# Kernel optimization log

Measured on AMD Instinct MI355X. Metric: run time of the kernel, lower is better.

Reference implementation:

```python
import jax, jax.numpy as jnp
import numpy as np

N, M, E, D = 100000, 20000, 1600000, 128


def setup_inputs() -> dict:
    key = jax.random.key(0)
    ks = jax.random.split(key, 14)
    s = 1.0 / np.sqrt(D)
    inp = {
        "x": jax.random.normal(ks[0], (N, D), jnp.float32),
        "in_src": jax.random.randint(ks[1], (E,), 0, N),
        "in_dst": jax.random.randint(ks[2], (E,), 0, M),
        "has_src": jax.random.randint(ks[3], (E,), 0, M),
        "has_dst": jax.random.randint(ks[4], (E,), 0, N),
        "W1": jax.random.normal(ks[5], (D, D), jnp.float32) * s,
        "b1": jnp.zeros((D,), jnp.float32),
        "an1": jax.random.normal(ks[6], (D, 1), jnp.float32) * s,
        "ae1": jax.random.normal(ks[7], (D, 1), jnp.float32) * s,
        "W2": jax.random.normal(ks[8], (D, D), jnp.float32) * s,
        "b2": jnp.zeros((D,), jnp.float32),
        "an2": jax.random.normal(ks[9], (D, 1), jnp.float32) * s,
        "ae2": jax.random.normal(ks[10], (D, 1), jnp.float32) * s,
    }
    return inp


def _hgat_layer(x, W, b, an, ae, in_src, in_dst, has_src, has_dst, activate):
    h = x @ W + b                       # [N, D] fc transform
    n_attn = h @ an                     # [N, 1] node attn scores
    # node -> hyperedge ('in' edges). h_e is unset at this point (local_scope),
    # so the hyperedge bias term is zero; e = attn[src].
    e = n_attn[in_src]                  # [E, 1]
    # source uses F.softmax(e, dim=0): GLOBAL softmax over all edges
    attn = jax.nn.softmax(e, axis=0)    # [E, 1]
    h_e = jax.ops.segment_sum(attn * h[in_src], in_dst, num_segments=M)  # [M, D]
    e_attn = h_e @ ae                   # [M, 1] hyperedge attn scores
    # hyperedge -> node ('has' edges): bias is node attn score at dst
    e2 = e_attn[has_src] + n_attn[has_dst]  # [E, 1]
    attn2 = jax.nn.softmax(e2, axis=0)      # global softmax over all edges
    h_n = jax.ops.segment_sum(attn2 * h_e[has_src], has_dst, num_segments=N)  # [N, D]
    return jax.nn.relu(h_n) if activate else h_n


def reference(x, in_src, in_dst, has_src, has_dst,
              W1, b1, an1, ae1, W2, b2, an2, ae2):
    # layer 1 (activation=relu), layer 2 (no activation); dropout in eval mode
    h = _hgat_layer(x, W1, b1, an1, ae1, in_src, in_dst, has_src, has_dst, True)
    h = _hgat_layer(h, W2, b2, an2, ae2, in_src, in_dst, has_src, has_dst, False)
    return h
```

## Files before the change

kernel.cpp:

```cpp
#include <hip/hip_runtime.h>
#include <hip/hip_bf16.h>
#include <math.h>
#include <type_traits>


typedef unsigned int u32;
typedef unsigned short u16;
typedef u16 u16x8 __attribute__((ext_vector_type(8)));
typedef short bf16x8 __attribute__((ext_vector_type(8)));
typedef float f32x4 __attribute__((ext_vector_type(4)));

#define NCONST 100000
#define MCONST 20000
#define ECONST 1600000
#define HCH2 32768
#define HBC 32
#define NCH_N 4

#define PBLK 256
#define PT 6250
#define SHB_IN 6
#define NBK_IN 313
#define SRCB_IN 17
#define SHB_HAS 8
#define NBK_HAS 391
#define SRCB_HAS 15

__device__ __forceinline__ u16 f2bf(float f) {
  u32 u = __float_as_uint(f);
  u += 0x7FFFu + ((u >> 16) & 1u);
  return (u16)(u >> 16);
}
__device__ __forceinline__ float bf2f(u16 b) {
  return __uint_as_float(((u32)b) << 16);
}

__global__ __launch_bounds__(256) void k_hpart2(const int* __restrict__ in_dst,
                                                const int* __restrict__ has_dst,
                                                const int* __restrict__ in_src,
                                                int* __restrict__ partial) {
  __shared__ int hc[HCH2];
  int y = blockIdx.y;
  const int* __restrict__ arr = (y == 0) ? in_dst : (y <= 4 ? has_dst : in_src);
  int lo = (y == 0) ? 0 : (y <= 4 ? (y - 1) * HCH2 : (y - 5) * HCH2);
  for (int i = threadIdx.x; i < HCH2; i += 256) hc[i] = 0;
  __syncthreads();
  int stride = gridDim.x * 256;
  int n4 = ECONST >> 2;
  const int4* a4 = (const int4*)arr;
  for (int i = blockIdx.x * 256 + threadIdx.x; i < n4; i += stride) {
    int4 v = a4[i];
    u32 a = (u32)(v.x - lo), b = (u32)(v.y - lo), c = (u32)(v.z - lo), d = (u32)(v.w - lo);
    if (a < HCH2) atomicAdd(&hc[a], 1);
    if (b < HCH2) atomicAdd(&hc[b], 1);
    if (c < HCH2) atomicAdd(&hc[c], 1);
    if (d < HCH2) atomicAdd(&hc[d], 1);
  }
  __syncthreads();
  int* out = partial + ((size_t)y * HBC + blockIdx.x) * HCH2;
  for (int i = threadIdx.x; i < HCH2; i += 256) out[i] = hc[i];
}

__global__ void k_scan1d(const int* __restrict__ partial, int nM, int nN,
                         int* __restrict__ off_in, int* __restrict__ off_has,
                         int* __restrict__ deg, int* __restrict__ bsum) {
  __shared__ int sd[256];
  int y = blockIdx.y;
  int n = y ? nN : nM;
  int rowbase = (y == 0) ? 0 : (y == 1 ? 1 : 5);
  int t = threadIdx.x;
  int base = blockIdx.x * 1024 + t * 4;
  int v[4];
#pragma unroll
  for (int k = 0; k < 4; ++k) {
    int j = base + k;
    int s = 0;
    if (j < n) {
      int chunk = j >> 15;
      int jl = j & (HCH2 - 1);
      const int* p = partial + ((size_t)(rowbase + chunk) * HBC) * HCH2 + jl;
#pragma unroll
      for (int b = 0; b < HBC; ++b) s += p[(size_t)b * HCH2];
    }
    v[k] = s;
  }
  if (y == 2) {
#pragma unroll
    for (int k = 0; k < 4; ++k)
      if (base + k < n) deg[base + k] = v[k];
    return;
  }
  int* off = y ? off_has : off_in;
  int* bs = bsum + y * 128;
  v[1] += v[0]; v[2] += v[1]; v[3] += v[2];
  int tot = v[3];
  sd[t] = tot;
  __syncthreads();
  for (int o = 1; o < 256; o <<= 1) {
    int x = (t >= o) ? sd[t - o] : 0;
    __syncthreads();
    sd[t] += x;
    __syncthreads();
  }
  int excl = sd[t] - tot;
#pragma unroll
  for (int k = 0; k < 4; ++k)
    if (base + k < n) off[base + k + 1] = v[k] + excl;
  if (t == 255) bs[blockIdx.x] = sd[255];
}

__global__ void k_scan2d(int* __restrict__ bsum, int nbM, int nbN) {
  __shared__ int sd[256];
  int* bs = bsum + blockIdx.x * 128;
  int nb = blockIdx.x ? nbN : nbM;
  int t = threadIdx.x;
  int v = (t < nb) ? bs[t] : 0;
  sd[t] = v;
  __syncthreads();
  for (int o = 1; o < 256; o <<= 1) {
    int x = (t >= o) ? sd[t - o] : 0;
    __syncthreads();
    sd[t] += x;
    __syncthreads();
  }
  if (t < nb) bs[t] = sd[t] - v;
}

__global__ void k_scan3d(int* __restrict__ off_in, int* __restrict__ off_has,
                         const int* __restrict__ bsum, int nM, int nN) {
  int y = blockIdx.y;
  int* off = y ? off_has : off_in;
  const int* bs = bsum + y * 128;
  int n = y ? nN : nM;
  int i = blockIdx.x * blockDim.x + threadIdx.x;
  int st = gridDim.x * blockDim.x;
  if (blockIdx.x == 0 && threadIdx.x == 0) off[0] = 0;
  for (; i < n; i += st) off[i + 1] += bs[i >> 10];
}

__global__ __launch_bounds__(256) void k_coarse(const int* __restrict__ in_dst,
                                                const int* __restrict__ has_dst,
                                                int* __restrict__ bb_in,
                                                int* __restrict__ bb_has) {
  __shared__ int h1[NBK_IN];
  __shared__ int h2[NBK_HAS];
  for (int i = threadIdx.x; i < NBK_IN; i += 256) h1[i] = 0;
  for (int i = threadIdx.x; i < NBK_HAS; i += 256) h2[i] = 0;
  __syncthreads();
  int c0 = blockIdx.x * PT, c1 = min(c0 + PT, ECONST);
  for (int i = c0 + threadIdx.x; i < c1; i += 256) {
    atomicAdd(&h1[in_dst[i] >> SHB_IN], 1);
    atomicAdd(&h2[has_dst[i] >> SHB_HAS], 1);
  }
  __syncthreads();
  int* o1 = bb_in + (size_t)blockIdx.x * NBK_IN;
  for (int i = threadIdx.x; i < NBK_IN; i += 256) o1[i] = h1[i];
  int* o2 = bb_has + (size_t)blockIdx.x * NBK_HAS;
  for (int i = threadIdx.x; i < NBK_HAS; i += 256) o2[i] = h2[i];
}

template <int NBUK, int SHB>
__device__ __forceinline__ void colscan_body(int* __restrict__ bb,
                                             const int* __restrict__ off, int segs,
                                             int* sd) {
  int b = blockIdx.x;
  if (b >= NBUK) return;
  int t = threadIdx.x;
  int v = bb[(size_t)t * NBUK + b];
  sd[t] = v;
  __syncthreads();
  for (int o = 1; o < 256; o <<= 1) {
    int x = (t >= o) ? sd[t - o] : 0;
    __syncthreads();
    sd[t] += x;
    __syncthreads();
  }
  bb[(size_t)t * NBUK + b] = sd[t] - v + off[min(b << SHB, segs)];
}

__global__ __launch_bounds__(256) void k_colscan2(int* __restrict__ bb_in,
                                                  const int* __restrict__ off_in,
                                                  int* __restrict__ bb_has,
                                                  const int* __restrict__ off_has) {
  __shared__ int sd[256];
  if (blockIdx.y == 0)
    colscan_body<NBK_IN, SHB_IN>(bb_in, off_in, MCONST, sd);
  else
    colscan_body<NBK_HAS, SHB_HAS>(bb_has, off_has, NCONST, sd);
}

template <int NBUK, int SHB, int SRCB>
__device__ __forceinline__ void stage_body(const int* __restrict__ dst,
                                           const int* __restrict__ srcv,
                                           const int* __restrict__ bb,
                                           int* __restrict__ ebuf, int* hist, int* loff,
                                           int* gbase, int* stg, int* sd) {
  int t = threadIdx.x;
  for (int i = t; i < NBUK; i += 256) hist[i] = 0;
  __syncthreads();
  int c0 = blockIdx.x * PT, c1 = min(c0 + PT, ECONST);
  for (int i = c0 + t; i < c1; i += 256) atomicAdd(&hist[dst[i] >> SHB], 1);
  __syncthreads();
  {
    int v0 = (2 * t < NBUK) ? hist[2 * t] : 0;
    int v1 = (2 * t + 1 < NBUK) ? hist[2 * t + 1] : 0;
    sd[t] = v0 + v1;
    __syncthreads();
    for (int o = 1; o < 256; o <<= 1) {
      int x = (t >= o) ? sd[t - o] : 0;
      __syncthreads();
      sd[t] += x;
      __syncthreads();
    }
    int excl = sd[t] - (v0 + v1);
    if (2 * t < NBUK) loff[2 * t] = excl;
    if (2 * t + 1 < NBUK) loff[2 * t + 1] = excl + v0;
  }
  __syncthreads();
  for (int i = t; i < NBUK; i += 256) {
    gbase[i] = bb[(size_t)blockIdx.x * NBUK + i];
    hist[i] = loff[i];
  }
  __syncthreads();
  for (int i = c0 + t; i < c1; i += 256) {
    int d = dst[i], s = srcv[i];
    int b = d >> SHB;
    int r = atomicAdd(&hist[b], 1);
    stg[r] = (b << 23) | ((d & ((1 << SHB) - 1)) << SRCB) | s;
  }
  __syncthreads();
  int tot = c1 - c0;
  for (int i = t; i < tot; i += 256) {
    int v = stg[i];
    int b = ((u32)v) >> 23;
    ebuf[gbase[b] + (i - loff[b])] = v & ((1 << 23) - 1);
  }
}

__global__ __launch_bounds__(256) void k_stage2(
    const int* __restrict__ in_dst, const int* __restrict__ in_src,
    const int* __restrict__ bb_in, int* __restrict__ ebuf_in,
    const int* __restrict__ has_dst, const int* __restrict__ has_src,
    const int* __restrict__ bb_has, int* __restrict__ ebuf_has) {
  __shared__ int hist[NBK_HAS];
  __shared__ int loff[NBK_HAS];
  __shared__ int gbase[NBK_HAS];
  __shared__ int stg[PT];
  __shared__ int sd[256];
  if (blockIdx.y == 0)
    stage_body<NBK_IN, SHB_IN, SRCB_IN>(in_dst, in_src, bb_in, ebuf_in, hist, loff, gbase,
                                        stg, sd);
  else
    stage_body<NBK_HAS, SHB_HAS, SRCB_HAS>(has_dst, has_src, bb_has, ebuf_has, hist, loff,
                                           gbase, stg, sd);
}

template <int SHB, int SRCB>
__device__ __forceinline__ void place_body(const int* __restrict__ off, int segs,
                                           const int* __restrict__ ebuf,
                                           int* __restrict__ csrc, int* cur) {
  const int NSEG = 1 << SHB;
  int seg0 = blockIdx.x << SHB;
  if (seg0 >= segs) return;
  int segN = min(seg0 + NSEG, segs);
  for (int i = threadIdx.x; i < segN - seg0; i += 256) cur[i] = off[seg0 + i];
  __syncthreads();
  int start = off[seg0], end = off[segN];
  for (int i = start + threadIdx.x; i < end; i += 256) {
    int v = ebuf[i];
    int dloc = ((u32)v) >> SRCB;
    int pos = atomicAdd(&cur[dloc], 1);
    csrc[pos] = v & ((1 << SRCB) - 1);
  }
}

__global__ __launch_bounds__(256) void k_place2(
    const int* __restrict__ off_in, const int* __restrict__ ebuf_in,
    int* __restrict__ csrc_in, const int* __restrict__ off_has,
    const int* __restrict__ ebuf_has, int* __restrict__ csrc_has) {
  __shared__ int cur[256];
  if (blockIdx.y == 0)
    place_body<SHB_IN, SRCB_IN>(off_in, MCONST, ebuf_in, csrc_in, cur);
  else
    place_body<SHB_HAS, SRCB_HAS>(off_has, NCONST, ebuf_has, csrc_has, cur);
}

__device__ __forceinline__ void merge_write(float m, float s, float2* __restrict__ pairs) {
  for (int o = 1; o < 64; o <<= 1) {
    float om = __shfl_xor(m, o, 64), os = __shfl_xor(s, o, 64);
    float nm = fmaxf(m, om);
    s = s * __expf(m - nm) + os * __expf(om - nm);
    m = nm;
  }
  __shared__ float sm[4], ss[4];
  int t = threadIdx.x;
  if ((t & 63) == 0) { sm[t >> 6] = m; ss[t >> 6] = s; }
  __syncthreads();
  if (t == 0) {
    for (int k = 1; k < 4; ++k) {
      float nm = fmaxf(m, sm[k]);
      s = s * __expf(m - nm) + ss[k] * __expf(sm[k] - nm);
      m = nm;
    }
    pairs[blockIdx.x] = make_float2(m, s);
  }
}

template <typename IT>
__global__ __launch_bounds__(256, 3) void k_fc(
    const IT* __restrict__ x, const float* __restrict__ W,
    const float* __restrict__ bias, const float* __restrict__ an,
    const int* __restrict__ deg, u16* __restrict__ h, float* __restrict__ na,
    float2* __restrict__ pairs, int nrows) {
  __shared__ __align__(16) u16 sWT[128 * 136];
  __shared__ float sNa[128];
  int tid = threadIdx.x;
  int lane = tid & 63, w = tid >> 6;
  int cl = lane & 15, qg = lane >> 4;

  for (int i = tid * 4; i < 16384; i += 1024) {
    float4 v = *(const float4*)(W + i);
    int k = i >> 7, j = i & 127;
    sWT[(j + 0) * 136 + k] = f2bf(v.x);
    sWT[(j + 1) * 136 + k] = f2bf(v.y);
    sWT[(j + 2) * 136 + k] = f2bf(v.z);
    sWT[(j + 3) * 136 + k] = f2bf(v.w);
  }

  float anv[8], bv[8];
#pragma unroll
  for (int t = 0; t < 8; ++t) {
    anv[t] = an[t * 16 + cl];
    bv[t] = bias[t * 16 + cl];
  }

  int rbase = blockIdx.x * 128 + w * 32;
  bf16x8 afr[2][4];
#pragma unroll
  for (int g = 0; g < 2; ++g) {
    int r = rbase + g * 16 + cl;
    int rc = min(r, nrows - 1);
    const IT* xp = x + (size_t)rc * 128 + qg * 8;
#pragma unroll
    for (int s = 0; s < 4; ++s) {
      if constexpr (sizeof(IT) == 4) {
        float4 u0 = *(const float4*)(xp + s * 32);
        float4 u1 = *(const float4*)(xp + s * 32 + 4);
        bf16x8 a;
        a[0] = (short)f2bf(u0.x); a[1] = (short)f2bf(u0.y);
        a[2] = (short)f2bf(u0.z); a[3] = (short)f2bf(u0.w);
        a[4] = (short)f2bf(u1.x); a[5] = (short)f2bf(u1.y);
        a[6] = (short)f2bf(u1.z); a[7] = (short)f2bf(u1.w);
        afr[g][s] = a;
      } else {
        afr[g][s] = *(const bf16x8*)(xp + s * 32);
      }
    }
  }
  __syncthreads();

  f32x4 acc[2][8];
#pragma unroll
  for (int g = 0; g < 2; ++g)
#pragma unroll
    for (int t = 0; t < 8; ++t) {
      acc[g][t][0] = 0.f; acc[g][t][1] = 0.f; acc[g][t][2] = 0.f; acc[g][t][3] = 0.f;
    }

#pragma unroll
  for (int t = 0; t < 8; ++t) {
    bf16x8 bfrg[4];
    const u16* bp = sWT + (t * 16 + cl) * 136 + qg * 8;
#pragma unroll
    for (int s = 0; s < 4; ++s) bfrg[s] = *(const bf16x8*)(bp + s * 32);
#pragma unroll
    for (int s = 0; s < 4; ++s) {
#pragma unroll
      for (int g = 0; g < 2; ++g)
        acc[g][t] = __builtin_amdgcn_mfma_f32_16x16x32_bf16(afr[g][s], bfrg[s], acc[g][t],
                                                            0, 0, 0);
    }
  }

  float pa[2][4];
#pragma unroll
  for (int g = 0; g < 2; ++g)
#pragma unroll
    for (int reg = 0; reg < 4; ++reg) pa[g][reg] = 0.f;
#pragma unroll
  for (int g = 0; g < 2; ++g)
#pragma unroll
    for (int t = 0; t < 8; ++t)
#pragma unroll
      for (int reg = 0; reg < 4; ++reg)
        pa[g][reg] = fmaf(acc[g][t][reg] + bv[t], anv[t], pa[g][reg]);
#pragma unroll
  for (int g = 0; g < 2; ++g)
#pragma unroll
    for (int reg = 0; reg < 4; ++reg) {
      float v = pa[g][reg];
      v += __shfl_xor(v, 1, 64);
      v += __shfl_xor(v, 2, 64);
      v += __shfl_xor(v, 4, 64);
      v += __shfl_xor(v, 8, 64);
      pa[g][reg] = v;
    }
  if (cl == 0) {
#pragma unroll
    for (int g = 0; g < 2; ++g)
#pragma unroll
      for (int reg = 0; reg < 4; ++reg) {
        int r = rbase + g * 16 + qg * 4 + reg;
        int lidx = w * 32 + g * 16 + qg * 4 + reg;
        if (r < nrows) {
          na[r] = pa[g][reg];
          sNa[lidx] = pa[g][reg];
        }
      }
  }

  __syncthreads();
  u16* st = sWT + w * 32 * 136;
#pragma unroll
  for (int g = 0; g < 2; ++g)
#pragma unroll
    for (int t = 0; t < 8; ++t)
#pragma unroll
      for (int reg = 0; reg < 4; ++reg)
        st[(g * 16 + qg * 4 + reg) * 136 + t * 16 + cl] = f2bf(acc[g][t][reg] + bv[t]);
#pragma unroll
  for (int it = 0; it < 8; ++it) {
    int idx = it * 64 + lane;
    int row = idx >> 4, c = idx & 15;
    u16x8 v = *(const u16x8*)(st + row * 136 + c * 8);
    int r = rbase + row;
    if (r < nrows) *(u16x8*)(h + (size_t)r * 128 + c * 8) = v;
  }

  float m1 = -1e30f, s1 = 0.f;
  if (tid < 128) {
    int r = blockIdx.x * 128 + tid;
    if (r < nrows) {
      int d = deg[r];
      if (d > 0) { m1 = sNa[tid]; s1 = (float)d; }
    }
  }
  merge_write(m1, s1, pairs);
}

__global__ void k_sm2(const float* __restrict__ ea, const float* __restrict__ na,
                      const int* __restrict__ hs, const int* __restrict__ hd, int n,
                      float2* __restrict__ pairs) {
  float m = -1e30f, s = 0.f;
  int i = blockIdx.x * blockDim.x + threadIdx.x;
  int st = gridDim.x * blockDim.x;
  for (; i < n; i += st) {
    float xv = ea[hs[i]] + na[hd[i]];
    if (xv > m) { s *= __expf(m - xv); m = xv; }
    s += __expf(xv - m);
  }
  merge_write(m, s, pairs);
}

__global__ void k_smfin(const float2* __restrict__ pairs, int nb, float* __restrict__ out) {
  int t = threadIdx.x;
  float m = -1e30f, s = 0.f;
  for (int i = t; i < nb; i += 256) {
    float2 pr = pairs[i];
    float nm = fmaxf(m, pr.x);
    s = s * __expf(m - nm) + pr.y * __expf(pr.x - nm);
    m = nm;
  }
  for (int o = 1; o < 64; o <<= 1) {
    float om = __shfl_xor(m, o, 64), os = __shfl_xor(s, o, 64);
    float nm = fmaxf(m, om);
    s = s * __expf(m - nm) + os * __expf(om - nm);
    m = nm;
  }
  __shared__ float sm[4], ss[4];
  if ((t & 63) == 0) { sm[t >> 6] = m; ss[t >> 6] = s; }
  __syncthreads();
  if (t == 0) {
    for (int k = 1; k < 4; ++k) {
      float nm = fmaxf(m, sm[k]);
      s = s * __expf(m - nm) + ss[k] * __expf(sm[k] - nm);
      m = nm;
    }
    out[0] = m;
    out[1] = s;
  }
}

__global__ __launch_bounds__(256) void k_segA(
    const u16* __restrict__ h, const float* __restrict__ na,
    const float* __restrict__ scal, const int* __restrict__ csrc,
    const int* __restrict__ off, const float* __restrict__ ae, u16* __restrict__ he,
    float* __restrict__ ea, int m_count) {
  int wid = (blockIdx.x << 2) + (threadIdx.x >> 6);
  if (wid >= m_count) return;
  float mx = scal[0];
  float iz = 1.0f / scal[1];
  int lane = threadIdx.x & 63;
  int sub = lane >> 4, cl = lane & 15;
  int s = off[wid], t = off[wid + 1];
  float ax[8];
#pragma unroll
  for (int j = 0; j < 8; ++j) ax[j] = 0.f;
  for (int i = s + sub; i < t; i += 4) {
    int sr = csrc[i];
    float ww = __expf(na[sr] - mx) * iz;
    u16x8 v = *(const u16x8*)(h + (size_t)sr * 128 + cl * 8);
#pragma unroll
    for (int j = 0; j < 8; ++j) ax[j] = fmaf(ww, bf2f(v[j]), ax[j]);
  }
#pragma unroll
  for (int j = 0; j < 8; ++j) {
    ax[j] += __shfl_xor(ax[j], 16, 64);
    ax[j] += __shfl_xor(ax[j], 32, 64);
  }
  float4 a0 = *(const float4*)(ae + cl * 8);
  float4 a1 = *(const float4*)(ae + cl * 8 + 4);
  float pa = ax[0] * a0.x + ax[1] * a0.y + ax[2] * a0.z + ax[3] * a0.w +
             ax[4] * a1.x + ax[5] * a1.y + ax[6] * a1.z + ax[7] * a1.w;
  pa += __shfl_xor(pa, 1, 64);
  pa += __shfl_xor(pa, 2, 64);
  pa += __shfl_xor(pa, 4, 64);
  pa += __shfl_xor(pa, 8, 64);
  if (sub == 0) {
    u16x8 o;
#pragma unroll
    for (int j = 0; j < 8; ++j) o[j] = f2bf(ax[j]);
    *(u16x8*)(he + (size_t)wid * 128 + cl * 8) = o;
    if (cl == 0) ea[wid] = pa;
  }
}

template <int L1>
__global__ __launch_bounds__(256) void k_segB(
    const u16* __restrict__ he, const float* __restrict__ ea,
    const float* __restrict__ na, const float* __restrict__ scal,
    const int* __restrict__ csrc, const int* __restrict__ off,
    void* __restrict__ yout, int n_count) {
  int wid = (blockIdx.x << 2) + (threadIdx.x >> 6);
  if (wid >= n_count) return;
  float mx2 = scal[2];
  float iz2 = 1.0f / scal[3];
  int lane = threadIdx.x & 63;
  int sub = lane >> 4, cl = lane & 15;
  float nav = na[wid];
  int s = off[wid], t = off[wid + 1];
  float ax[8];
#pragma unroll
  for (int j = 0; j < 8; ++j) ax[j] = 0.f;
  for (int i = s + sub; i < t; i += 4) {
    int sr = csrc[i];
    float c = __expf(ea[sr] + nav - mx2) * iz2;
    u16x8 v = *(const u16x8*)(he + (size_t)sr * 128 + cl * 8);
#pragma unroll
    for (int j = 0; j < 8; ++j) ax[j] = fmaf(c, bf2f(v[j]), ax[j]);
  }
#pragma unroll
  for (int j = 0; j < 8; ++j) {
    ax[j] += __shfl_xor(ax[j], 16, 64);
    ax[j] += __shfl_xor(ax[j], 32, 64);
    if (L1) ax[j] = fmaxf(ax[j], 0.f);
  }
  if (sub == 0) {
    if (L1) {
      u16x8 o;
#pragma unroll
      for (int j = 0; j < 8; ++j) o[j] = f2bf(ax[j]);
      *(u16x8*)((u16*)yout + (size_t)wid * 128 + cl * 8) = o;
    } else {
      float4 A = make_float4(ax[0], ax[1], ax[2], ax[3]);
      float4 B = make_float4(ax[4], ax[5], ax[6], ax[7]);
      float* y = (float*)yout;
      *(float4*)(y + (size_t)wid * 128 + cl * 8) = A;
      *(float4*)(y + (size_t)wid * 128 + cl * 8 + 4) = B;
    }
  }
}

extern "C" void kernel_launch(void* const* d_in, const int* in_sizes, int n_in,
                              void* d_out, int out_size, void* d_ws, size_t ws_size,
                              hipStream_t stream) {
  const int N = NCONST, M = MCONST, E = ECONST;
  const float* x = (const float*)d_in[0];
  const int* in_src = (const int*)d_in[1];
  const int* in_dst = (const int*)d_in[2];
  const int* has_src = (const int*)d_in[3];
  const int* has_dst = (const int*)d_in[4];
  const float* W1 = (const float*)d_in[5];
  const float* b1 = (const float*)d_in[6];
  const float* an1 = (const float*)d_in[7];
  const float* ae1 = (const float*)d_in[8];
  const float* W2 = (const float*)d_in[9];
  const float* b2 = (const float*)d_in[10];
  const float* an2 = (const float*)d_in[11];
  const float* ae2 = (const float*)d_in[12];

  const size_t PARTIAL_BYTES = (size_t)9 * HBC * HCH2 * 4;

  char* p = (char*)d_ws;
  auto alloc = [&](size_t bytes) {
    char* q = p;
    p += (bytes + 255) & ~(size_t)255;
    return q;
  };
  u16* h = (u16*)alloc((size_t)N * 128 * 2);
  u16* he = (u16*)alloc((size_t)M * 128 * 2);
  float* na = (float*)alloc((size_t)N * 4);
  float* ea = (float*)alloc((size_t)M * 4);
  int* deg = (int*)alloc((size_t)N * 4);
  int* off_in = (int*)alloc((size_t)(M + 1) * 4);
  int* off_has = (int*)alloc((size_t)(N + 1) * 4);
  int* csrc_in = (int*)alloc((size_t)E * 4);
  int* csrc_has = (int*)alloc((size_t)E * 4);
  int* partial = (int*)alloc(PARTIAL_BYTES);
  int* ebuf_in = partial;
  int* ebuf_has = partial + ECONST;
  int* bb_in = (int*)alloc((size_t)PBLK * NBK_IN * 4);
  int* bb_has = (int*)alloc((size_t)PBLK * NBK_HAS * 4);
  int* bsum = (int*)alloc(256 * 4);
  float2* pairs = (float2*)alloc(1024 * 8);
  float* scal = (float*)alloc(64);
  if ((size_t)(p - (char*)d_ws) > ws_size) return;

  u16* y1b = (u16*)d_out;

  k_hpart2<<<dim3(HBC, 9), 256, 0, stream>>>(in_dst, has_dst, in_src, partial);
  int nbM = (M + 1023) / 1024, nbN = (N + 1023) / 1024;
  k_scan1d<<<dim3(nbN, 3), 256, 0, stream>>>(partial, M, N, off_in, off_has, deg, bsum);
  k_scan2d<<<2, 256, 0, stream>>>(bsum, nbM, nbN);
  k_scan3d<<<dim3(512, 2), 256, 0, stream>>>(off_in, off_has, bsum, M, N);

  k_coarse<<<PBLK, 256, 0, stream>>>(in_dst, has_dst, bb_in, bb_has);
  k_colscan2<<<dim3(NBK_HAS, 2), 256, 0, stream>>>(bb_in, off_in, bb_has, off_has);
  k_stage2<<<dim3(PBLK, 2), 256, 0, stream>>>(in_dst, in_src, bb_in, ebuf_in, has_dst,
                                              has_src, bb_has, ebuf_has);
  k_place2<<<dim3(NBK_HAS, 2), 256, 0, stream>>>(off_in, ebuf_in, csrc_in, off_has,
                                                 ebuf_has, csrc_has);

  const int FCB = (N + 127) / 128;
  auto layer = [&](auto xin, const float* W, const float* b, const float* an_,
                   const float* ae_, auto seg_b) {
    using IT = typename std::remove_const<
        typename std::remove_pointer<decltype(xin)>::type>::type;
    k_fc<IT><<<FCB, 256, 0, stream>>>(xin, W, b, an_, deg, h, na, pairs, N);
    k_smfin<<<1, 256, 0, stream>>>(pairs, FCB, scal);
    k_segA<<<(M + 3) / 4, 256, 0, stream>>>(h, na, scal, csrc_in, off_in, ae_, he, ea, M);
    k_sm2<<<256, 256, 0, stream>>>(ea, na, has_src, has_dst, E, pairs);
    k_smfin<<<1, 256, 0, stream>>>(pairs, 256, scal + 2);
    seg_b();
  };

  layer((const float*)x, W1, b1, an1, ae1, [&] {
    k_segB<1><<<(N + 3) / 4, 256, 0, stream>>>(he, ea, na, scal, csrc_has, off_has,
                                               (void*)y1b, N);
  });
  layer((const u16*)y1b, W2, b2, an2, ae2, [&] {
    k_segB<0><<<(N + 3) / 4, 256, 0, stream>>>(he, ea, na, scal, csrc_has, off_has,
                                               d_out, N);
  });
}
```

Baseline: 471.0 us.

## Defer layer-1 softmax normalization and split hyperedge aggregation across column slices

Layer 1's second global softmax pass is removed. Layer 1 now accumulates unnormalized exp weights (no max subtraction) and sums them inside segB. The 1/Z factor is folded into layer 2's fc input, which is valid because relu commutes with a positive scale. Node weights are precomputed once per node, and the node-to-hyperedge aggregation is split into 8 column slices with 32 edges in flight per wave. The hyperedge attention dot product moves to its own small kernel, and layer 2's softmax stats are computed over the CSR layout instead of the raw edge list. Skipping the max subtraction risks overflow for large scores and adds bf16 rounding when rescaling the inputs.

```diff
diff --git a/kernel.cpp b/kernel.cpp
--- a/kernel.cpp
+++ b/kernel.cpp
@@ -15,7 +15,6 @@
 #define ECONST 1600000
 #define HCH2 32768
 #define HBC 32
-#define NCH_N 4
 
 #define PBLK 256
 #define PT 6250
@@ -306,17 +305,18 @@
   }
 }
 
-template <typename IT>
+template <typename IT, bool SCALE>
 __global__ __launch_bounds__(256, 3) void k_fc(
     const IT* __restrict__ x, const float* __restrict__ W,
     const float* __restrict__ bias, const float* __restrict__ an,
-    const int* __restrict__ deg, u16* __restrict__ h, float* __restrict__ na,
-    float2* __restrict__ pairs, int nrows) {
+    const int* __restrict__ deg, const float* __restrict__ scal_c,
+    u16* __restrict__ h, float* __restrict__ na, float2* __restrict__ pairs, int nrows) {
   __shared__ __align__(16) u16 sWT[128 * 136];
   __shared__ float sNa[128];
   int tid = threadIdx.x;
   int lane = tid & 63, w = tid >> 6;
   int cl = lane & 15, qg = lane >> 4;
+  float C = SCALE ? scal_c[4] : 1.0f;
 
   for (int i = tid * 4; i < 16384; i += 1024) {
     float4 v = *(const float4*)(W + i);
@@ -353,7 +353,12 @@
         a[6] = (short)f2bf(u1.z); a[7] = (short)f2bf(u1.w);
         afr[g][s] = a;
       } else {
-        afr[g][s] = *(const bf16x8*)(xp + s * 32);
+        bf16x8 a = *(const bf16x8*)(xp + s * 32);
+        if constexpr (SCALE) {
+#pragma unroll
+          for (int j = 0; j < 8; ++j) a[j] = (short)f2bf(bf2f((u16)a[j]) * C);
+        }
+        afr[g][s] = a;
       }
     }
   }
@@ -448,20 +453,6 @@
   merge_write(m1, s1, pairs);
 }
 
-__global__ void k_sm2(const float* __restrict__ ea, const float* __restrict__ na,
-                      const int* __restrict__ hs, const int* __restrict__ hd, int n,
-                      float2* __restrict__ pairs) {
-  float m = -1e30f, s = 0.f;
-  int i = blockIdx.x * blockDim.x + threadIdx.x;
-  int st = gridDim.x * blockDim.x;
-  for (; i < n; i += st) {
-    float xv = ea[hs[i]] + na[hd[i]];
-    if (xv > m) { s *= __expf(m - xv); m = xv; }
-    s += __expf(xv - m);
-  }
-  merge_write(m, s, pairs);
-}
-
 __global__ void k_smfin(const float2* __restrict__ pairs, int nb, float* __restrict__ out) {
   int t = threadIdx.x;
   float m = -1e30f, s = 0.f;
@@ -491,48 +482,97 @@
   }
 }
 
-__global__ __launch_bounds__(256) void k_segA(
-    const u16* __restrict__ h, const float* __restrict__ na,
-    const float* __restrict__ scal, const int* __restrict__ csrc,
-    const int* __restrict__ off, const float* __restrict__ ae, u16* __restrict__ he,
-    float* __restrict__ ea, int m_count) {
-  int wid = (blockIdx.x << 2) + (threadIdx.x >> 6);
+__global__ __launch_bounds__(256) void k_wnode(const float* __restrict__ na,
+                                               const float* __restrict__ scal,
+                                               float* __restrict__ wn, int n) {
+  int i = blockIdx.x * 256 + threadIdx.x;
+  if (i < n) wn[i] = __expf(na[i] - scal[0]) * (1.0f / scal[1]);
+}
+
+__global__ __launch_bounds__(256) void k_segAs(
+    const u16* __restrict__ h, const float* __restrict__ wn,
+    const int* __restrict__ csrc, const int* __restrict__ off,
+    u16* __restrict__ he, int m_count) {
+  int bid = blockIdx.x;
+  int slice = bid & 7;
+  int wid = (bid >> 3) * 4 + (threadIdx.x >> 6);
   if (wid >= m_count) return;
-  float mx = scal[0];
-  float iz = 1.0f / scal[1];
   int lane = threadIdx.x & 63;
-  int sub = lane >> 4, cl = lane & 15;
+  int eslot = lane >> 1, ch = lane & 1;
+  int col = slice * 16 + ch * 8;
   int s = off[wid], t = off[wid + 1];
   float ax[8];
 #pragma unroll
   for (int j = 0; j < 8; ++j) ax[j] = 0.f;
-  for (int i = s + sub; i < t; i += 4) {
+  for (int i = s + eslot; i < t; i += 32) {
     int sr = csrc[i];
-    float ww = __expf(na[sr] - mx) * iz;
-    u16x8 v = *(const u16x8*)(h + (size_t)sr * 128 + cl * 8);
+    float ww = wn[sr];
+    u16x8 v = *(const u16x8*)(h + (size_t)sr * 128 + col);
 #pragma unroll
     for (int j = 0; j < 8; ++j) ax[j] = fmaf(ww, bf2f(v[j]), ax[j]);
   }
 #pragma unroll
   for (int j = 0; j < 8; ++j) {
+    ax[j] += __shfl_xor(ax[j], 2, 64);
+    ax[j] += __shfl_xor(ax[j], 4, 64);
+    ax[j] += __shfl_xor(ax[j], 8, 64);
     ax[j] += __shfl_xor(ax[j], 16, 64);
     ax[j] += __shfl_xor(ax[j], 32, 64);
   }
+  if (eslot == 0) {
+    u16x8 o;
+#pragma unroll
+    for (int j = 0; j < 8; ++j) o[j] = f2bf(ax[j]);
+    *(u16x8*)(he + (size_t)wid * 128 + col) = o;
+  }
+}
+
+__global__ __launch_bounds__(256) void k_ea(const u16* __restrict__ he,
+                                            const float* __restrict__ ae,
+                                            float* __restrict__ ea, int m) {
+  int row = blockIdx.x * 16 + (threadIdx.x >> 4);
+  int cl = threadIdx.x & 15;
+  if (row >= m) return;
+  u16x8 v = *(const u16x8*)(he + (size_t)row * 128 + cl * 8);
   float4 a0 = *(const float4*)(ae + cl * 8);
   float4 a1 = *(const float4*)(ae + cl * 8 + 4);
-  float pa = ax[0] * a0.x + ax[1] * a0.y + ax[2] * a0.z + ax[3] * a0.w +
-             ax[4] * a1.x + ax[5] * a1.y + ax[6] * a1.z + ax[7] * a1.w;
+  float pa = bf2f(v[0]) * a0.x + bf2f(v[1]) * a0.y + bf2f(v[2]) * a0.z +
+             bf2f(v[3]) * a0.w + bf2f(v[4]) * a1.x + bf2f(v[5]) * a1.y +
+             bf2f(v[6]) * a1.z + bf2f(v[7]) * a1.w;
   pa += __shfl_xor(pa, 1, 64);
   pa += __shfl_xor(pa, 2, 64);
   pa += __shfl_xor(pa, 4, 64);
   pa += __shfl_xor(pa, 8, 64);
-  if (sub == 0) {
-    u16x8 o;
-#pragma unroll
-    for (int j = 0; j < 8; ++j) o[j] = f2bf(ax[j]);
-    *(u16x8*)(he + (size_t)wid * 128 + cl * 8) = o;
-    if (cl == 0) ea[wid] = pa;
-  }
+  if (cl == 0) ea[row] = pa;
+}
+
+__global__ void k_sm2c(const float* __restrict__ na, const float* __restrict__ ea,
+                       const int* __restrict__ csrc, const int* __restrict__ off, int n,
+                       float2* __restrict__ pairs) {
+  float m = -1e30f, s = 0.f;
+  int gid = blockIdx.x * 256 + threadIdx.x;
+  int stride = gridDim.x * 256;
+  for (int i = gid; i < n; i += stride) {
+    float nav = na[i];
+    int a = off[i], b = off[i + 1];
+    for (int j = a; j < b; ++j) {
+      float xv = nav + ea[csrc[j]];
+      if (xv > m) { s *= __expf(m - xv); m = xv; }
+      s += __expf(xv - m);
+    }
+  }
+  merge_write(m, s, pairs);
+}
+
+__global__ void k_s2fin(const float2* __restrict__ pairs, int nb, float* __restrict__ out) {
+  int t = threadIdx.x;
+  float s = 0.f;
+  for (int i = t; i < nb; i += 256) s += pairs[i].x;
+  for (int o = 1; o < 64; o <<= 1) s += __shfl_xor(s, o, 64);
+  __shared__ float sm[4];
+  if ((t & 63) == 0) sm[t >> 6] = s;
+  __syncthreads();
+  if (t == 0) out[4] = 1.0f / (sm[0] + sm[1] + sm[2] + sm[3]);
 }
 
 template <int L1>
@@ -540,44 +580,56 @@
     const u16* __restrict__ he, const float* __restrict__ ea,
     const float* __restrict__ na, const float* __restrict__ scal,
     const int* __restrict__ csrc, const int* __restrict__ off,
-    void* __restrict__ yout, int n_count) {
-  int wid = (blockIdx.x << 2) + (threadIdx.x >> 6);
-  if (wid >= n_count) return;
-  float mx2 = scal[2];
-  float iz2 = 1.0f / scal[3];
+    void* __restrict__ yout, float2* __restrict__ pairs, int n_count) {
+  __shared__ float swv[4];
+  int wv = threadIdx.x >> 6;
+  int wid = (blockIdx.x << 2) + wv;
   int lane = threadIdx.x & 63;
   int sub = lane >> 4, cl = lane & 15;
-  float nav = na[wid];
-  int s = off[wid], t = off[wid + 1];
-  float ax[8];
-#pragma unroll
-  for (int j = 0; j < 8; ++j) ax[j] = 0.f;
-  for (int i = s + sub; i < t; i += 4) {
-    int sr = csrc[i];
-    float c = __expf(ea[sr] + nav - mx2) * iz2;
-    u16x8 v = *(const u16x8*)(he + (size_t)sr * 128 + cl * 8);
-#pragma unroll
-    for (int j = 0; j < 8; ++j) ax[j] = fmaf(c, bf2f(v[j]), ax[j]);
-  }
-#pragma unroll
-  for (int j = 0; j < 8; ++j) {
-    ax[j] += __shfl_xor(ax[j], 16, 64);
-    ax[j] += __shfl_xor(ax[j], 32, 64);
-    if (L1) ax[j] = fmaxf(ax[j], 0.f);
-  }
-  if (sub == 0) {
-    if (L1) {
-      u16x8 o;
-#pragma unroll
-      for (int j = 0; j < 8; ++j) o[j] = f2bf(ax[j]);
-      *(u16x8*)((u16*)yout + (size_t)wid * 128 + cl * 8) = o;
-    } else {
-      float4 A = make_float4(ax[0], ax[1], ax[2], ax[3]);
-      float4 B = make_float4(ax[4], ax[5], ax[6], ax[7]);
-      float* y = (float*)yout;
-      *(float4*)(y + (size_t)wid * 128 + cl * 8) = A;
-      *(float4*)(y + (size_t)wid * 128 + cl * 8 + 4) = B;
-    }
+  float sx = 0.f;
+  if (wid < n_count) {
+    float mx2 = L1 ? 0.f : scal[2];
+    float iz2 = L1 ? 1.f : (1.0f / scal[3]);
+    float nav = na[wid];
+    int s = off[wid], t = off[wid + 1];
+    float ax[8];
+#pragma unroll
+    for (int j = 0; j < 8; ++j) ax[j] = 0.f;
+    for (int i = s + sub; i < t; i += 4) {
+      int sr = csrc[i];
+      float c = __expf(ea[sr] + nav - mx2) * iz2;
+      if (L1 && cl == 0) sx += c;
+      u16x8 v = *(const u16x8*)(he + (size_t)sr * 128 + cl * 8);
+#pragma unroll
+      for (int j = 0; j < 8; ++j) ax[j] = fmaf(c, bf2f(v[j]), ax[j]);
+    }
+#pragma unroll
+    for (int j = 0; j < 8; ++j) {
+      ax[j] += __shfl_xor(ax[j], 16, 64);
+      ax[j] += __shfl_xor(ax[j], 32, 64);
+      if (L1) ax[j] = fmaxf(ax[j], 0.f);
+    }
+    if (sub == 0) {
+      if (L1) {
+        u16x8 o;
+#pragma unroll
+        for (int j = 0; j < 8; ++j) o[j] = f2bf(ax[j]);
+        *(u16x8*)((u16*)yout + (size_t)wid * 128 + cl * 8) = o;
+      } else {
+        float4 A = make_float4(ax[0], ax[1], ax[2], ax[3]);
+        float4 B = make_float4(ax[4], ax[5], ax[6], ax[7]);
+        float* y = (float*)yout;
+        *(float4*)(y + (size_t)wid * 128 + cl * 8) = A;
+        *(float4*)(y + (size_t)wid * 128 + cl * 8 + 4) = B;
+      }
+    }
+  }
+  if (L1) {
+    for (int o = 1; o < 64; o <<= 1) sx += __shfl_xor(sx, o, 64);
+    if (lane == 0) swv[wv] = sx;
+    __syncthreads();
+    if (threadIdx.x == 0)
+      pairs[blockIdx.x] = make_float2(swv[0] + swv[1] + swv[2] + swv[3], 0.f);
   }
 }
 
@@ -611,6 +663,7 @@
   u16* he = (u16*)alloc((size_t)M * 128 * 2);
   float* na = (float*)alloc((size_t)N * 4);
   float* ea = (float*)alloc((size_t)M * 4);
+  float* wn = (float*)alloc((size_t)N * 4);
   int* deg = (int*)alloc((size_t)N * 4);
   int* off_in = (int*)alloc((size_t)(M + 1) * 4);
   int* off_has = (int*)alloc((size_t)(N + 1) * 4);
@@ -622,7 +675,7 @@
   int* bb_in = (int*)alloc((size_t)PBLK * NBK_IN * 4);
   int* bb_has = (int*)alloc((size_t)PBLK * NBK_HAS * 4);
   int* bsum = (int*)alloc(256 * 4);
-  float2* pairs = (float2*)alloc(1024 * 8);
+  float2* pairs = (float2*)alloc((size_t)25600 * 8);
   float* scal = (float*)alloc(64);
   if ((size_t)(p - (char*)d_ws) > ws_size) return;
 
@@ -642,24 +695,24 @@
                                                  ebuf_has, csrc_has);
 
   const int FCB = (N + 127) / 128;
-  auto layer = [&](auto xin, const float* W, const float* b, const float* an_,
-                   const float* ae_, auto seg_b) {
-    using IT = typename std::remove_const<
-        typename std::remove_pointer<decltype(xin)>::type>::type;
-    k_fc<IT><<<FCB, 256, 0, stream>>>(xin, W, b, an_, deg, h, na, pairs, N);
-    k_smfin<<<1, 256, 0, stream>>>(pairs, FCB, scal);
-    k_segA<<<(M + 3) / 4, 256, 0, stream>>>(h, na, scal, csrc_in, off_in, ae_, he, ea, M);
-    k_sm2<<<256, 256, 0, stream>>>(ea, na, has_src, has_dst, E, pairs);
-    k_smfin<<<1, 256, 0, stream>>>(pairs, 256, scal + 2);
-    seg_b();
-  };
-
-  layer((const float*)x, W1, b1, an1, ae1, [&] {
-    k_segB<1><<<(N + 3) / 4, 256, 0, stream>>>(he, ea, na, scal, csrc_has, off_has,
-                                               (void*)y1b, N);
-  });
-  layer((const u16*)y1b, W2, b2, an2, ae2, [&] {
-    k_segB<0><<<(N + 3) / 4, 256, 0, stream>>>(he, ea, na, scal, csrc_has, off_has,
-                                               d_out, N);
-  });
-}
+  const int SAB = ((M + 3) / 4) * 8;
+  const int SBB = (N + 3) / 4;
+
+  k_fc<float, false><<<FCB, 256, 0, stream>>>(x, W1, b1, an1, deg, scal, h, na, pairs, N);
+  k_smfin<<<1, 256, 0, stream>>>(pairs, FCB, scal);
+  k_wnode<<<(N + 255) / 256, 256, 0, stream>>>(na, scal, wn, N);
+  k_segAs<<<SAB, 256, 0, stream>>>(h, wn, csrc_in, off_in, he, M);
+  k_ea<<<(M + 15) / 16, 256, 0, stream>>>(he, ae1, ea, M);
+  k_segB<1><<<SBB, 256, 0, stream>>>(he, ea, na, scal, csrc_has, off_has, (void*)y1b,
+                                     pairs, N);
+  k_s2fin<<<1, 256, 0, stream>>>(pairs, SBB, scal);
+
+  k_fc<u16, true><<<FCB, 256, 0, stream>>>(y1b, W2, b2, an2, deg, scal, h, na, pairs, N);
+  k_smfin<<<1, 256, 0, stream>>>(pairs, FCB, scal);
+  k_wnode<<<(N + 255) / 256, 256, 0, stream>>>(na, scal, wn, N);
+  k_segAs<<<SAB, 256, 0, stream>>>(h, wn, csrc_in, off_in, he, M);
+  k_ea<<<(M + 15) / 16, 256, 0, stream>>>(he, ae2, ea, M);
+  k_sm2c<<<128, 256, 0, stream>>>(na, ea, csrc_has, off_has, N, pairs);
+  k_smfin<<<1, 256, 0, stream>>>(pairs, 128, scal + 2);
+  k_segB<0><<<SBB, 256, 0, stream>>>(he, ea, na, scal, csrc_has, off_has, d_out, pairs, N);
+}
```

After: 735.8 us. +56.2%, slower.
